# Kernel optimization log

Hardware: AMD Instinct MI355X
Metric: run time of the kernel (lower is better)

## Reference

```python
import jax, jax.numpy as jnp
import numpy as np


def squash(s, axis=-1):
    sq = jnp.sum(jnp.square(s), axis=axis, keepdims=True)
    scale = sq / (1.0 + sq) / (jnp.sqrt(sq) + 1e-08)
    return scale * s


def setup_inputs() -> dict:
    key = jax.random.key(0)
    k1, k2 = jax.random.split(key)
    # [B, input_num_caps, input_dim_caps]
    x = jax.random.normal(k1, (64, 1152, 8), dtype=jnp.float32)
    # W: [input_num_caps, num_capsules, input_dim_caps, dim_capsules]
    W = jax.random.normal(k2, (1152, 32, 8, 16), dtype=jnp.float32) * 0.05
    return {"x": x, "W": W}


def reference(x, W):
    # Original tiles x along the output-capsule axis before the einsum
    # 'bicd,icde->bice'; since the tiled copies are identical along c,
    # this is exactly 'bid,icde->bice' without materializing the tile.
    u_hat = jnp.einsum('bid,icde->bice', x, W)  # [B, I, C, E]
    b = jnp.zeros(u_hat.shape[:3], dtype=u_hat.dtype)  # [B, I, C]
    routings = 3
    v = None
    for i in range(routings):
        c = jax.nn.softmax(b, axis=-1)                 # over output capsules
        s = jnp.einsum('bic,bice->bce', c, u_hat)      # weighted sum over I
        v = squash(s)                                  # [B, C, E]
        if i < routings - 1:
            b = b + jnp.einsum('bice,bce->bic', u_hat, v)  # agreement
    return v
```

## Files before the change

### kernel.cpp

```cpp
#include <hip/hip_runtime.h>
#include <hip/hip_fp16.h>

#define B_ 64
#define I_ 1152
#define C_ 32
#define E_ 16
#define D_ 8
#define BC_ 8
#define ICt 12
#define NIC (I_/ICt)
#define ICX (NIC/8)
#define WROW4 (C_*D_*E_/4)
#define SCE (B_*C_*E_)
#define SCE2 (SCE/2)

__device__ __forceinline__ void gload_lds16(const void* g, void* l) {
  typedef __attribute__((address_space(1))) const void GV;
  typedef __attribute__((address_space(3))) void LV;
  __builtin_amdgcn_global_load_lds((GV*)g, (LV*)l, 16, 0, 0);
}

#define WAITVM(N) do { asm volatile("s_waitcnt vmcnt(" #N ")" ::: "memory"); \
                       __builtin_amdgcn_sched_barrier(0); } while (0)
#define WAITLG0()  do { asm volatile("s_waitcnt lgkmcnt(0)" ::: "memory");   \
                       __builtin_amdgcn_sched_barrier(0); } while (0)

template<bool ROUTE>
__global__ __launch_bounds__(256)
void caps_pass(const float* __restrict__ x, const float* __restrict__ W,
               const float* __restrict__ vacc, __half* __restrict__ partial)
{
  __shared__ float4 Wl[3][C_*32];
  __shared__ float4 xl[BC_*ICt*2];

  const int t   = threadIdx.x;
  const int c   = t & 31;
  const int eh  = (t >> 5) & 1;
  const int bq  = t >> 6;
  const int xcd = blockIdx.x & 7;
  const int sl  = blockIdx.x >> 3;
  const int ic  = xcd * ICX + (sl >> 3);
  const int b0  = (sl & 7) * BC_;
  const int i0  = ic * ICt;

  int fsrc[4];
#pragma unroll
  for (int k = 0; k < 4; ++k) {
    int cc = (t >> 5) + 8*k;
    fsrc[k] = cc*32 + ((c - cc) & 31);
  }

  float vr[2][8];
  if (ROUTE) {
#pragma unroll
    for (int j = 0; j < 2; ++j) {
      const float4* vp = (const float4*)(vacc + (((size_t)(b0 + bq*2 + j)*C_ + c)*E_ + eh*8));
      float4 a = vp[0], b = vp[1];
      vr[j][0]=a.x; vr[j][1]=a.y; vr[j][2]=a.z; vr[j][3]=a.w;
      vr[j][4]=b.x; vr[j][5]=b.y; vr[j][6]=b.z; vr[j][7]=b.w;
    }
  }

  if (t < BC_*ICt*2) {
    int b = t / (ICt*2), r = t % (ICt*2);
    xl[t] = ((const float4*)x)[ ((size_t)(b0 + b)*I_ + i0)*2 + r ];
  }

  const float4* wg = (const float4*)(W + (size_t)i0 * (C_*D_*E_));
#pragma unroll
  for (int k = 0; k < 4; ++k) gload_lds16(wg + fsrc[k],          &Wl[0][t + 256*k]);
#pragma unroll
  for (int k = 0; k < 4; ++k) gload_lds16(wg + WROW4 + fsrc[k],  &Wl[1][t + 256*k]);

  float acc[2][8];
#pragma unroll
  for (int j = 0; j < 2; ++j)
#pragma unroll
    for (int e = 0; e < 8; ++e) acc[j][e] = 0.f;

  int cur = 0;
  for (int ii = 0; ii < ICt; ++ii) {
    WAITLG0();
    __builtin_amdgcn_s_barrier();
    __builtin_amdgcn_sched_barrier(0);

    if (ii + 2 < ICt) {
      int pre = cur + 2; if (pre >= 3) pre -= 3;
      const float4* wn = wg + (size_t)(ii + 2) * WROW4;
#pragma unroll
      for (int k = 0; k < 4; ++k)
        gload_lds16(wn + fsrc[k], &Wl[pre][t + 256*k]);
    }

    if (ii < ICt - 2)       WAITVM(8);
    else if (ii == ICt - 2) WAITVM(4);
    else                    WAITVM(0);
    __builtin_amdgcn_s_barrier();
    __builtin_amdgcn_sched_barrier(0);

    float xv[2][8];
#pragma unroll
    for (int j = 0; j < 2; ++j) {
      float4 a = xl[(bq*2 + j)*(ICt*2) + ii*2 + 0];
      float4 b = xl[(bq*2 + j)*(ICt*2) + ii*2 + 1];
      xv[j][0]=a.x; xv[j][1]=a.y; xv[j][2]=a.z; xv[j][3]=a.w;
      xv[j][4]=b.x; xv[j][5]=b.y; xv[j][6]=b.z; xv[j][7]=b.w;
    }

    float uh[2][8];
#pragma unroll
    for (int j = 0; j < 2; ++j)
#pragma unroll
      for (int e = 0; e < 8; ++e) uh[j][e] = 0.f;

#pragma unroll
    for (int d = 0; d < D_; ++d) {
#pragma unroll
      for (int qq = 0; qq < 2; ++qq) {
        float4 wv = Wl[cur][c*32 + (((d*4 + eh*2 + qq) + c) & 31)];
        const int eb = qq*4;
#pragma unroll
        for (int j = 0; j < 2; ++j) {
          uh[j][eb+0] = fmaf(xv[j][d], wv.x, uh[j][eb+0]);
          uh[j][eb+1] = fmaf(xv[j][d], wv.y, uh[j][eb+1]);
          uh[j][eb+2] = fmaf(xv[j][d], wv.z, uh[j][eb+2]);
          uh[j][eb+3] = fmaf(xv[j][d], wv.w, uh[j][eb+3]);
        }
      }
    }

    float coef[2];
    if (ROUTE) {
#pragma unroll
      for (int j = 0; j < 2; ++j) {
        float lg = 0.f;
#pragma unroll
        for (int e = 0; e < 8; ++e) lg = fmaf(uh[j][e], vr[j][e], lg);
        lg += __shfl_xor(lg, 32, 64);
        float p = __expf(lg);
        float s = p;
#pragma unroll
        for (int mk = 16; mk >= 1; mk >>= 1) s += __shfl_xor(s, mk, 64);
        coef[j] = p * __builtin_amdgcn_rcpf(s);
      }
    } else {
#pragma unroll
      for (int j = 0; j < 2; ++j) coef[j] = (1.0f / C_);
    }

#pragma unroll
    for (int j = 0; j < 2; ++j)
#pragma unroll
      for (int e = 0; e < 8; ++e) acc[j][e] = fmaf(coef[j], uh[j][e], acc[j][e]);

    cur = (cur + 1 == 3) ? 0 : cur + 1;
  }

#pragma unroll
  for (int j = 0; j < 2; ++j) {
    size_t base = ((size_t)ic * B_ + (b0 + bq*2 + j)) * (C_*E_) + (size_t)c*E_ + eh*8;
    __half2 h0 = __float22half2_rn({acc[j][0], acc[j][1]});
    __half2 h1 = __float22half2_rn({acc[j][2], acc[j][3]});
    __half2 h2 = __float22half2_rn({acc[j][4], acc[j][5]});
    __half2 h3 = __float22half2_rn({acc[j][6], acc[j][7]});
    __half2* dst = (__half2*)(partial + base);
    dst[0] = h0; dst[1] = h1; dst[2] = h2; dst[3] = h3;
  }
}

__global__ __launch_bounds__(256)
void reduce_squash(const __half2* __restrict__ partial, float* __restrict__ vacc,
                   float* __restrict__ out, int mode)
{
  __shared__ float2 sm[256];
  const int t    = threadIdx.x;
  const int pair = blockIdx.x*64 + (t & 63);
  const int part = t >> 6;
  const __half2* p = partial + (size_t)(part*(NIC/4)) * SCE2 + pair;
  float2 s = {0.f, 0.f};
#pragma unroll 6
  for (int k = 0; k < NIC/4; ++k) {
    float2 f = __half22float2(p[(size_t)k * SCE2]);
    s.x += f.x; s.y += f.y;
  }
  sm[t] = s;
  __syncthreads();
  if (t < 64) {
    float2 a = sm[t], b = sm[t+64], c2 = sm[t+128], d = sm[t+192];
    float2 tot = {a.x+b.x+c2.x+d.x, a.y+b.y+c2.y+d.y};
    float sq = tot.x*tot.x + tot.y*tot.y;
    sq += __shfl_xor(sq, 1); sq += __shfl_xor(sq, 2); sq += __shfl_xor(sq, 4);
    float scale = sq / (1.f + sq) / (sqrtf(sq) + 1e-8f);
    float vx = scale * tot.x, vy = scale * tot.y;
    const int cell = pair * 2;
    if (mode == 0)      { vacc[cell] = vx;  vacc[cell+1] = vy;  }
    else if (mode == 1) { vacc[cell] += vx; vacc[cell+1] += vy; }
    else                { out[cell]  = vx;  out[cell+1]  = vy;  }
  }
}

extern "C" void kernel_launch(void* const* d_in, const int* in_sizes, int n_in,
                              void* d_out, int out_size, void* d_ws, size_t ws_size,
                              hipStream_t stream)
{
  const float* x = (const float*)d_in[0];
  const float* W = (const float*)d_in[1];
  float* out     = (float*)d_out;

  __half* partial = (__half*)d_ws;
  float*  vacc    = (float*)((char*)d_ws + (size_t)NIC*SCE*sizeof(__half));

  dim3 pg(NIC * (B_/BC_));
  const int rg = SCE2 / 64;

  caps_pass<false><<<pg, 256, 0, stream>>>(x, W, nullptr, partial);
  reduce_squash<<<rg, 256, 0, stream>>>((const __half2*)partial, vacc, nullptr, 0);
  caps_pass<true ><<<pg, 256, 0, stream>>>(x, W, vacc, partial);
  reduce_squash<<<rg, 256, 0, stream>>>((const __half2*)partial, vacc, nullptr, 1);
  caps_pass<true ><<<pg, 256, 0, stream>>>(x, W, vacc, partial);
  reduce_squash<<<rg, 256, 0, stream>>>((const __half2*)partial, vacc, out, 2);
}
```

Baseline: 73.99 us.

## Convert W and x to fp16 once and compute routing passes with packed half math

Adds a conversion kernel that turns W into fp16 and x into duplicated half2 pairs. The three routing passes then stream half as much W data and use packed half FMAs and fdot2 for u_hat, the agreement logits and the accumulation. LDS layout changes to an XOR-swizzled 256-byte row per capsule. This targets W bandwidth and ALU cost in the three passes, but adds an extra conversion launch over W each call and accumulates in fp16, which risks accuracy loss over 12-step partial sums.

```diff
diff --git a/kernel.cpp b/kernel.cpp
--- a/kernel.cpp
+++ b/kernel.cpp
@@ -10,9 +10,9 @@
 #define ICt 12
 #define NIC (I_/ICt)
 #define ICX (NIC/8)
-#define WROW4 (C_*D_*E_/4)
 #define SCE (B_*C_*E_)
 #define SCE2 (SCE/2)
+#define WIB 8192
 
 __device__ __forceinline__ void gload_lds16(const void* g, void* l) {
   typedef __attribute__((address_space(1))) const void GV;
@@ -20,18 +20,70 @@
   __builtin_amdgcn_global_load_lds((GV*)g, (LV*)l, 16, 0, 0);
 }
 
-#define WAITVM(N) do { asm volatile("s_waitcnt vmcnt(" #N ")" ::: "memory"); \
-                       __builtin_amdgcn_sched_barrier(0); } while (0)
-#define WAITLG0()  do { asm volatile("s_waitcnt lgkmcnt(0)" ::: "memory");   \
-                       __builtin_amdgcn_sched_barrier(0); } while (0)
+#define WAITVM4() do { asm volatile("s_waitcnt vmcnt(4)" ::: "memory"); \
+                       __builtin_amdgcn_sched_barrier(0); } while (0)
+#define WAITVM2() do { asm volatile("s_waitcnt vmcnt(2)" ::: "memory"); \
+                       __builtin_amdgcn_sched_barrier(0); } while (0)
+#define WAITVM0() do { asm volatile("s_waitcnt vmcnt(0)" ::: "memory"); \
+                       __builtin_amdgcn_sched_barrier(0); } while (0)
+#define WAITLG0() do { asm volatile("s_waitcnt lgkmcnt(0)" ::: "memory"); \
+                       __builtin_amdgcn_sched_barrier(0); } while (0)
+
+typedef _Float16 h2v __attribute__((ext_vector_type(2)));
+
+__device__ __forceinline__ float dot2f(__half2 a, __half2 b, float c) {
+#if defined(__has_builtin)
+#if __has_builtin(__builtin_amdgcn_fdot2)
+  return __builtin_amdgcn_fdot2(__builtin_bit_cast(h2v, a),
+                                __builtin_bit_cast(h2v, b), c, false);
+#else
+  float2 fa = __half22float2(a), fb = __half22float2(b);
+  return fmaf(fa.x, fb.x, fmaf(fa.y, fb.y, c));
+#endif
+#else
+  float2 fa = __half22float2(a), fb = __half22float2(b);
+  return fmaf(fa.x, fb.x, fmaf(fa.y, fb.y, c));
+#endif
+}
+
+__global__ __launch_bounds__(256)
+void convert_wx(const float* __restrict__ W, const float* __restrict__ x,
+                __half* __restrict__ Wh, __half2* __restrict__ xh)
+{
+  const int bid = blockIdx.x;
+  const int t   = threadIdx.x;
+  if (bid < 2304) {
+    int G = bid*256 + t;
+    const float4* src = (const float4*)(W + (size_t)G*8);
+    float4 a = src[0], b = src[1];
+    __half2 h0 = __float22half2_rn({a.x, a.y});
+    __half2 h1 = __float22half2_rn({a.z, a.w});
+    __half2 h2 = __float22half2_rn({b.x, b.y});
+    __half2 h3 = __float22half2_rn({b.z, b.w});
+    float4 o;
+    o.x = __builtin_bit_cast(float, h0); o.y = __builtin_bit_cast(float, h1);
+    o.z = __builtin_bit_cast(float, h2); o.w = __builtin_bit_cast(float, h3);
+    *(float4*)(Wh + (size_t)G*8) = o;
+  } else {
+    int k = (bid - 2304)*256 + t;
+    const float4* src = (const float4*)(x + (size_t)k*4);
+    float4 a = src[0];
+    float4 o;
+    o.x = __builtin_bit_cast(float, __float22half2_rn({a.x, a.x}));
+    o.y = __builtin_bit_cast(float, __float22half2_rn({a.y, a.y}));
+    o.z = __builtin_bit_cast(float, __float22half2_rn({a.z, a.z}));
+    o.w = __builtin_bit_cast(float, __float22half2_rn({a.w, a.w}));
+    *(float4*)(xh + (size_t)k*4) = o;
+  }
+}
 
 template<bool ROUTE>
 __global__ __launch_bounds__(256)
-void caps_pass(const float* __restrict__ x, const float* __restrict__ W,
+void caps_pass(const __half2* __restrict__ xh, const char* __restrict__ Wh,
                const float* __restrict__ vacc, __half* __restrict__ partial)
 {
-  __shared__ float4 Wl[3][C_*32];
-  __shared__ float4 xl[BC_*ICt*2];
+  __shared__ float4 Wl[3][512];
+  __shared__ __half2 xl[BC_*ICt*D_];
 
   const int t   = threadIdx.x;
   const int c   = t & 31;
@@ -43,40 +95,43 @@
   const int b0  = (sl & 7) * BC_;
   const int i0  = ic * ICt;
 
-  int fsrc[4];
-#pragma unroll
-  for (int k = 0; k < 4; ++k) {
-    int cc = (t >> 5) + 8*k;
-    fsrc[k] = cc*32 + ((c - cc) & 31);
-  }
-
-  float vr[2][8];
+  int fsrc[2];
+#pragma unroll
+  for (int k = 0; k < 2; ++k) {
+    int g = t + 256*k, cc = g >> 4, q = g & 15;
+    fsrc[k] = cc*256 + ((q ^ (cc & 15)) << 4);
+  }
+
+  __half2 vrp[2][4];
   if (ROUTE) {
 #pragma unroll
     for (int j = 0; j < 2; ++j) {
       const float4* vp = (const float4*)(vacc + (((size_t)(b0 + bq*2 + j)*C_ + c)*E_ + eh*8));
       float4 a = vp[0], b = vp[1];
-      vr[j][0]=a.x; vr[j][1]=a.y; vr[j][2]=a.z; vr[j][3]=a.w;
-      vr[j][4]=b.x; vr[j][5]=b.y; vr[j][6]=b.z; vr[j][7]=b.w;
-    }
-  }
-
-  if (t < BC_*ICt*2) {
-    int b = t / (ICt*2), r = t % (ICt*2);
-    xl[t] = ((const float4*)x)[ ((size_t)(b0 + b)*I_ + i0)*2 + r ];
-  }
-
-  const float4* wg = (const float4*)(W + (size_t)i0 * (C_*D_*E_));
-#pragma unroll
-  for (int k = 0; k < 4; ++k) gload_lds16(wg + fsrc[k],          &Wl[0][t + 256*k]);
-#pragma unroll
-  for (int k = 0; k < 4; ++k) gload_lds16(wg + WROW4 + fsrc[k],  &Wl[1][t + 256*k]);
-
-  float acc[2][8];
+      vrp[j][0] = __float22half2_rn({a.x, a.y});
+      vrp[j][1] = __float22half2_rn({a.z, a.w});
+      vrp[j][2] = __float22half2_rn({b.x, b.y});
+      vrp[j][3] = __float22half2_rn({b.z, b.w});
+    }
+  }
+
+  if (t < BC_*ICt*D_/4) {
+    int b = t / 24, r = t % 24;
+    float4 v = ((const float4*)(xh + ((size_t)(b0 + b)*I_ + i0)*D_))[r];
+    ((float4*)xl)[b*24 + r] = v;
+  }
+
+  const char* wg = Wh + (size_t)i0 * WIB;
+#pragma unroll
+  for (int k = 0; k < 2; ++k) gload_lds16(wg + fsrc[k],        (char*)&Wl[0][0] + (t + 256*k)*16);
+#pragma unroll
+  for (int k = 0; k < 2; ++k) gload_lds16(wg + WIB + fsrc[k],  (char*)&Wl[1][0] + (t + 256*k)*16);
+
+  __half2 accp[2][4];
 #pragma unroll
   for (int j = 0; j < 2; ++j)
 #pragma unroll
-    for (int e = 0; e < 8; ++e) acc[j][e] = 0.f;
+    for (int q = 0; q < 4; ++q) accp[j][q] = __half2{__half(0.f), __half(0.f)};
 
   int cur = 0;
   for (int ii = 0; ii < ICt; ++ii) {
@@ -86,47 +141,43 @@
 
     if (ii + 2 < ICt) {
       int pre = cur + 2; if (pre >= 3) pre -= 3;
-      const float4* wn = wg + (size_t)(ii + 2) * WROW4;
-#pragma unroll
-      for (int k = 0; k < 4; ++k)
-        gload_lds16(wn + fsrc[k], &Wl[pre][t + 256*k]);
-    }
-
-    if (ii < ICt - 2)       WAITVM(8);
-    else if (ii == ICt - 2) WAITVM(4);
-    else                    WAITVM(0);
+      const char* wn = wg + (size_t)(ii + 2) * WIB;
+#pragma unroll
+      for (int k = 0; k < 2; ++k)
+        gload_lds16(wn + fsrc[k], (char*)&Wl[pre][0] + (t + 256*k)*16);
+    }
+
+    if (ii < ICt - 2)       WAITVM4();
+    else if (ii == ICt - 2) WAITVM2();
+    else                    WAITVM0();
     __builtin_amdgcn_s_barrier();
     __builtin_amdgcn_sched_barrier(0);
 
-    float xv[2][8];
-#pragma unroll
-    for (int j = 0; j < 2; ++j) {
-      float4 a = xl[(bq*2 + j)*(ICt*2) + ii*2 + 0];
-      float4 b = xl[(bq*2 + j)*(ICt*2) + ii*2 + 1];
-      xv[j][0]=a.x; xv[j][1]=a.y; xv[j][2]=a.z; xv[j][3]=a.w;
-      xv[j][4]=b.x; xv[j][5]=b.y; xv[j][6]=b.z; xv[j][7]=b.w;
-    }
-
-    float uh[2][8];
+    __half2 uhp[2][4];
 #pragma unroll
     for (int j = 0; j < 2; ++j)
 #pragma unroll
-      for (int e = 0; e < 8; ++e) uh[j][e] = 0.f;
-
+      for (int q = 0; q < 4; ++q) uhp[j][q] = __half2{__half(0.f), __half(0.f)};
+
+    const char* wrow = (const char*)&Wl[cur][0] + c*256;
+    const __half2* xr0 = xl + (bq*2 + 0)*(ICt*D_) + ii*D_;
+    const __half2* xr1 = xl + (bq*2 + 1)*(ICt*D_) + ii*D_;
 #pragma unroll
     for (int d = 0; d < D_; ++d) {
-#pragma unroll
-      for (int qq = 0; qq < 2; ++qq) {
-        float4 wv = Wl[cur][c*32 + (((d*4 + eh*2 + qq) + c) & 31)];
-        const int eb = qq*4;
-#pragma unroll
-        for (int j = 0; j < 2; ++j) {
-          uh[j][eb+0] = fmaf(xv[j][d], wv.x, uh[j][eb+0]);
-          uh[j][eb+1] = fmaf(xv[j][d], wv.y, uh[j][eb+1]);
-          uh[j][eb+2] = fmaf(xv[j][d], wv.z, uh[j][eb+2]);
-          uh[j][eb+3] = fmaf(xv[j][d], wv.w, uh[j][eb+3]);
-        }
-      }
+      float4 w4 = *(const float4*)(wrow + ((((d*2 + eh) ^ (c & 15))) << 4));
+      __half2 w0 = __builtin_bit_cast(__half2, w4.x);
+      __half2 w1 = __builtin_bit_cast(__half2, w4.y);
+      __half2 w2 = __builtin_bit_cast(__half2, w4.z);
+      __half2 w3 = __builtin_bit_cast(__half2, w4.w);
+      __half2 x0 = xr0[d], x1 = xr1[d];
+      uhp[0][0] = __hfma2(x0, w0, uhp[0][0]);
+      uhp[0][1] = __hfma2(x0, w1, uhp[0][1]);
+      uhp[0][2] = __hfma2(x0, w2, uhp[0][2]);
+      uhp[0][3] = __hfma2(x0, w3, uhp[0][3]);
+      uhp[1][0] = __hfma2(x1, w0, uhp[1][0]);
+      uhp[1][1] = __hfma2(x1, w1, uhp[1][1]);
+      uhp[1][2] = __hfma2(x1, w2, uhp[1][2]);
+      uhp[1][3] = __hfma2(x1, w3, uhp[1][3]);
     }
 
     float coef[2];
@@ -135,7 +186,7 @@
       for (int j = 0; j < 2; ++j) {
         float lg = 0.f;
 #pragma unroll
-        for (int e = 0; e < 8; ++e) lg = fmaf(uh[j][e], vr[j][e], lg);
+        for (int q = 0; q < 4; ++q) lg = dot2f(uhp[j][q], vrp[j][q], lg);
         lg += __shfl_xor(lg, 32, 64);
         float p = __expf(lg);
         float s = p;
@@ -149,9 +200,11 @@
     }
 
 #pragma unroll
-    for (int j = 0; j < 2; ++j)
-#pragma unroll
-      for (int e = 0; e < 8; ++e) acc[j][e] = fmaf(coef[j], uh[j][e], acc[j][e]);
+    for (int j = 0; j < 2; ++j) {
+      __half2 cp = __float2half2_rn(coef[j]);
+#pragma unroll
+      for (int q = 0; q < 4; ++q) accp[j][q] = __hfma2(cp, uhp[j][q], accp[j][q]);
+    }
 
     cur = (cur + 1 == 3) ? 0 : cur + 1;
   }
@@ -159,12 +212,12 @@
 #pragma unroll
   for (int j = 0; j < 2; ++j) {
     size_t base = ((size_t)ic * B_ + (b0 + bq*2 + j)) * (C_*E_) + (size_t)c*E_ + eh*8;
-    __half2 h0 = __float22half2_rn({acc[j][0], acc[j][1]});
-    __half2 h1 = __float22half2_rn({acc[j][2], acc[j][3]});
-    __half2 h2 = __float22half2_rn({acc[j][4], acc[j][5]});
-    __half2 h3 = __float22half2_rn({acc[j][6], acc[j][7]});
-    __half2* dst = (__half2*)(partial + base);
-    dst[0] = h0; dst[1] = h1; dst[2] = h2; dst[3] = h3;
+    float4 o;
+    o.x = __builtin_bit_cast(float, accp[j][0]);
+    o.y = __builtin_bit_cast(float, accp[j][1]);
+    o.z = __builtin_bit_cast(float, accp[j][2]);
+    o.w = __builtin_bit_cast(float, accp[j][3]);
+    *(float4*)(partial + base) = o;
   }
 }
 
@@ -207,16 +260,21 @@
   const float* W = (const float*)d_in[1];
   float* out     = (float*)d_out;
 
-  __half* partial = (__half*)d_ws;
-  float*  vacc    = (float*)((char*)d_ws + (size_t)NIC*SCE*sizeof(__half));
+  char* ws = (char*)d_ws;
+  __half*  partial = (__half*)ws;                    ws += (size_t)NIC*SCE*2;
+  float*   vacc    = (float*)ws;                     ws += (size_t)SCE*4;
+  __half*  Wh      = (__half*)ws;                    ws += (size_t)I_*C_*D_*E_*2;
+  __half2* xh      = (__half2*)ws;
 
   dim3 pg(NIC * (B_/BC_));
   const int rg = SCE2 / 64;
 
-  caps_pass<false><<<pg, 256, 0, stream>>>(x, W, nullptr, partial);
+  convert_wx<<<2880, 256, 0, stream>>>(W, x, Wh, xh);
+
+  caps_pass<false><<<pg, 256, 0, stream>>>(xh, (const char*)Wh, nullptr, partial);
   reduce_squash<<<rg, 256, 0, stream>>>((const __half2*)partial, vacc, nullptr, 0);
-  caps_pass<true ><<<pg, 256, 0, stream>>>(x, W, vacc, partial);
+  caps_pass<true ><<<pg, 256, 0, stream>>>(xh, (const char*)Wh, vacc, partial);
   reduce_squash<<<rg, 256, 0, stream>>>((const __half2*)partial, vacc, nullptr, 1);
-  caps_pass<true ><<<pg, 256, 0, stream>>>(x, W, vacc, partial);
+  caps_pass<true ><<<pg, 256, 0, stream>>>(xh, (const char*)Wh, vacc, partial);
   reduce_squash<<<rg, 256, 0, stream>>>((const __half2*)partial, vacc, out, 2);
 }
```

Result: no change. 73.87 us (-0.2%).
